# Performance work log

Hardware: AMD Instinct MI355X
Metric: run time of the kernel (lower is better)

## Reference

```python
import jax, jax.numpy as jnp
import numpy as np

NH = 16  # matches init kwarg nh


def setup_inputs() -> dict:
    key = jax.random.key(0)
    k1, k2 = jax.random.split(key)
    b, S, T = 4, 4096, 4096
    x = jax.random.normal(k1, (b, S, 1), dtype=jnp.float32)
    coords_rel = jax.random.normal(k2, (2, b, S, T), dtype=jnp.float32)
    return {"x": x, "coords_rel": coords_rel}


def reference(x, coords_rel):
    # coords_rel: [2, b, S, T]; x: [b, S, 1]
    d = jnp.sqrt(coords_rel[0] ** 2 + coords_rel[1] ** 2)            # [b, S, T]
    # torch.topk(d, NH, dim=1, largest=False): smallest NH along source dim, ascending
    neg_vals, idx = jax.lax.top_k(jnp.transpose(-d, (0, 2, 1)), NH)  # [b, T, NH]
    dist_abs = jnp.transpose(-neg_vals, (0, 2, 1))                   # [b, NH, T]
    indices = jnp.transpose(idx, (0, 2, 1))                          # [b, NH, T]
    b, nh, t = dist_abs.shape
    w = 1.0 / (dist_abs + 1e-15) ** 2                                # [b, nh, t]
    denom = w.sum(axis=2)                                            # [b, nh] (sum over t, as in source)
    # faithful reproduction of torch .view(t,b,nh) raw reinterpretation + broadcast divide + .view(b,t,nh)
    w = (w.reshape(t, b, nh) / denom).reshape(b, t, nh)              # [b, t, nh]
    S = x.shape[1]
    idx_btn = indices.reshape(b, t, nh)                              # raw reshape, matches torch .view
    # gather: out[i,j,k] = x[i, idx[i,j,k], 0]  (x.repeat over last dim makes all columns equal)
    xg = jnp.take_along_axis(jnp.broadcast_to(x, (b, S, nh)), idx_btn, axis=1)  # [b, t, nh]
    out = (xg * w).sum(axis=2)                                       # [b, t]
    return out[..., None]                                            # [b, t, 1]
```

## Files before the change

kernel.cpp:

```cpp
#include <hip/hip_runtime.h>

#define B_ 4
#define S_ 4096
#define T_ 4096
#define NH_ 16
#define CPB 32
#define CPW 2
#define ROWS 64
#define NTILE (S_ / ROWS)
#define LDSP 33
#define NCG (T_ / CPB)

typedef unsigned long long u64;

__global__ __launch_bounds__(1024, 8) void topk_scan(
    const float* __restrict__ coords,
    float* __restrict__ outW,
    int*   __restrict__ outI,
    float* __restrict__ partials)
{
    __shared__ float lds[2][2][ROWS * LDSP];
    __shared__ float red[16 * NH_];

    const int bid  = blockIdx.x;
    const int b    = bid >> 7;
    const int c0   = (bid & (NCG - 1)) * CPB;
    const int tid  = threadIdx.x;
    const int w    = tid >> 6;
    const int lane = tid & 63;

    const size_t plane = (size_t)B_ * S_ * T_;
    const int stid = tid & 511;
    const int srow = stid >> 3;
    const int scol = (stid & 7) * 4;
    const int pl   = (tid >= 512) ? 1 : 0;
    const float* gp = coords + (size_t)b * S_ * T_ + (size_t)srow * T_ + (c0 + scol)
                    + (pl ? plane : (size_t)0);
    float* w0 = &lds[0][pl][srow * LDSP + scol];
    float* w1 = &lds[1][pl][srow * LDSP + scol];

    float lv[CPW]; int li[CPW]; float tau[CPW];
#pragma unroll
    for (int cc = 0; cc < CPW; ++cc) {
        lv[cc]  = __int_as_float(0x7f800000);
        li[cc]  = 0;
        tau[cc] = __int_as_float(0x7f800000);
    }

    float4 r4 = *(const float4*)gp;
    w0[0] = r4.x; w0[1] = r4.y; w0[2] = r4.z; w0[3] = r4.w;
    r4 = *(const float4*)(gp + (size_t)ROWS * T_);
    __syncthreads();

#pragma unroll 1
    for (int k = 0; k < NTILE; ++k) {
        if (k + 1 < NTILE) {
            float* wb = (k & 1) ? w0 : w1;
            wb[0] = r4.x; wb[1] = r4.y; wb[2] = r4.z; wb[3] = r4.w;
        }
        if (k + 2 < NTILE)
            r4 = *(const float4*)(gp + (size_t)(k + 2) * ROWS * T_);

        const float* rb0 = lds[k & 1][0];
        const float* rb1 = lds[k & 1][1];
#pragma unroll
        for (int cc = 0; cc < CPW; ++cc) {
            const int col = w * CPW + cc;
            const float dx = rb0[lane * LDSP + col];
            const float dy = rb1[lane * LDSP + col];
            const float d2 = __fadd_rn(__fmul_rn(dx, dx), __fmul_rn(dy, dy));
            u64 m = __ballot(d2 < tau[cc]);
            while (m) {
                const int src = __ffsll(m) - 1;
                m &= m - 1;
                const float cd = __shfl(d2, src);
                const int   ci = k * ROWS + src;
                const unsigned pm = (unsigned)__ballot(lv[cc] <= cd) & 0xFFFFu;
                const int p = __popc(pm);
                const float uv = __shfl_up(lv[cc], 1);
                const int   ui = __shfl_up(li[cc], 1);
                const bool here  = (lane == p);
                const bool shift = (lane > p) && (lane < NH_);
                lv[cc] = here ? cd : (shift ? uv : lv[cc]);
                li[cc] = here ? ci : (shift ? ui : li[cc]);
                tau[cc] = __shfl(lv[cc], NH_ - 1);
                m &= __ballot(d2 < tau[cc]);
            }
        }
        __syncthreads();
    }

    float dsum = 0.f;
#pragma unroll
    for (int cc = 0; cc < CPW; ++cc) {
        const int t = c0 + w * CPW + cc;
        if (lane < NH_) {
            const float d = sqrtf(lv[cc]) + 1e-15f;
            const float wv = 1.0f / (d * d);
            outW[((size_t)b * T_ + t) * NH_ + lane] = wv;
            outI[((size_t)b * T_ + t) * NH_ + lane] = li[cc];
            dsum += wv;
        }
    }
    if (lane < NH_) red[w * NH_ + lane] = dsum;
    __syncthreads();
    if (tid < NH_) {
        float s = 0.f;
#pragma unroll
        for (int q = 0; q < 16; ++q) s += red[q * NH_ + tid];
        partials[(size_t)bid * NH_ + tid] = s;
    }
}

__global__ __launch_bounds__(128) void denom_reduce(
    const float* __restrict__ partials, float* __restrict__ denom)
{
    const int q = blockIdx.x;
    const int b = q >> 4, j = q & 15;
    const int g = threadIdx.x;
    __shared__ float sm[128];
    sm[g] = partials[(size_t)(b * NCG + g) * NH_ + j];
    __syncthreads();
    for (int s = 64; s > 0; s >>= 1) {
        if (g < s) sm[g] += sm[g + s];
        __syncthreads();
    }
    if (g == 0) denom[q] = sm[0];
}

__global__ __launch_bounds__(256) void out_kernel(
    const float* __restrict__ x,
    const float* __restrict__ outW,
    const int*   __restrict__ outI,
    const float* __restrict__ denom,
    float* __restrict__ out)
{
    const int gid = blockIdx.x * 256 + threadIdx.x;
    const int i = gid >> 12;
    const int j = gid & 4095;
    const int ih = j >> 8;
    const size_t base = ((size_t)i * T_ + (size_t)(j & 255) * NH_) * NH_ + ih;
    const int dq = (j & 3) * NH_;
    float acc = 0.f;
#pragma unroll
    for (int k = 0; k < NH_; ++k) {
        float w  = outW[base + (size_t)k * NH_];
        int   id = outI[base + (size_t)k * NH_];
        acc += x[i * S_ + id] * w / denom[dq + k];
    }
    out[gid] = acc;
}

extern "C" void kernel_launch(void* const* d_in, const int* in_sizes, int n_in,
                              void* d_out, int out_size, void* d_ws, size_t ws_size,
                              hipStream_t stream) {
    const float* x      = (const float*)d_in[0];
    const float* coords = (const float*)d_in[1];
    float* out = (float*)d_out;

    float* outW     = (float*)d_ws;
    int*   outI     = (int*)(outW + (size_t)B_ * T_ * NH_);
    float* partials = (float*)(outI + (size_t)B_ * T_ * NH_);
    float* denom    = partials + (size_t)(B_ * NCG) * NH_;

    topk_scan   <<<B_ * NCG,      1024, 0, stream>>>(coords, outW, outI, partials);
    denom_reduce<<<64,            128,  0, stream>>>(partials, denom);
    out_kernel  <<<B_ * T_ / 256, 256,  0, stream>>>(x, outW, outI, denom, out);
}
```

Baseline: 152.1 us.

## Stream coordinate tiles into LDS via direct global_load_lds with 4-buffer pipeline

Replaces the register-staged double-buffered copy of coordinate tiles with direct global-to-LDS loads (global_load_lds), using a 4-deep ring buffer and prefetch distance of two tiles with explicit vmcnt waits. The padded LDS layout is replaced with an XOR-swizzled layout to avoid bank conflicts, and one barrier per iteration is removed. It aims to cut VGPR staging traffic and hide global load latency, but it relies on the ring depth and a single barrier for correctness, and it raises LDS use per block.

```diff
diff --git a/kernel.cpp b/kernel.cpp
--- a/kernel.cpp
+++ b/kernel.cpp
@@ -7,11 +7,13 @@
 #define CPB 32
 #define CPW 2
 #define ROWS 64
-#define NTILE (S_ / ROWS)
-#define LDSP 33
+#define NT (S_ / ROWS)
+#define NBUF 4
 #define NCG (T_ / CPB)
 
 typedef unsigned long long u64;
+typedef const float __attribute__((address_space(1)))* gas1f;
+typedef float __attribute__((address_space(3)))* las3f;
 
 __global__ __launch_bounds__(1024, 8) void topk_scan(
     const float* __restrict__ coords,
@@ -19,7 +21,7 @@
     int*   __restrict__ outI,
     float* __restrict__ partials)
 {
-    __shared__ float lds[2][2][ROWS * LDSP];
+    __shared__ float lds[NBUF * 2 * ROWS * CPB];
     __shared__ float red[16 * NH_];
 
     const int bid  = blockIdx.x;
@@ -30,14 +32,10 @@
     const int lane = tid & 63;
 
     const size_t plane = (size_t)B_ * S_ * T_;
-    const int stid = tid & 511;
-    const int srow = stid >> 3;
-    const int scol = (stid & 7) * 4;
-    const int pl   = (tid >= 512) ? 1 : 0;
-    const float* gp = coords + (size_t)b * S_ * T_ + (size_t)srow * T_ + (c0 + scol)
-                    + (pl ? plane : (size_t)0);
-    float* w0 = &lds[0][pl][srow * LDSP + scol];
-    float* w1 = &lds[1][pl][srow * LDSP + scol];
+    const int srow   = ((w & 7) << 3) + (lane >> 3);
+    const int schunk = (lane & 7) ^ (lane >> 3);
+    const float* gtile = coords + (size_t)(w >> 3) * plane
+                       + ((size_t)b * S_ + srow) * T_ + (c0 + schunk * 4);
 
     float lv[CPW]; int li[CPW]; float tau[CPW];
 #pragma unroll
@@ -47,27 +45,32 @@
         tau[cc] = __int_as_float(0x7f800000);
     }
 
-    float4 r4 = *(const float4*)gp;
-    w0[0] = r4.x; w0[1] = r4.y; w0[2] = r4.z; w0[3] = r4.w;
-    r4 = *(const float4*)(gp + (size_t)ROWS * T_);
-    __syncthreads();
+#define ISSUE(kk) do {                                                         \
+    const float* gsrc_ = gtile + (size_t)(kk) * ROWS * T_;                     \
+    las3f ldst_ = (las3f)((char*)lds + (((kk) & 3) << 14) + (w << 10));        \
+    __builtin_amdgcn_global_load_lds((gas1f)gsrc_, ldst_, 16, 0, 0);           \
+} while (0)
+
+    ISSUE(0);
+    ISSUE(1);
 
 #pragma unroll 1
-    for (int k = 0; k < NTILE; ++k) {
-        if (k + 1 < NTILE) {
-            float* wb = (k & 1) ? w0 : w1;
-            wb[0] = r4.x; wb[1] = r4.y; wb[2] = r4.z; wb[3] = r4.w;
-        }
-        if (k + 2 < NTILE)
-            r4 = *(const float4*)(gp + (size_t)(k + 2) * ROWS * T_);
+    for (int k = 0; k < NT; ++k) {
+        if (k + 2 < NT) ISSUE(k + 2);
+        if (k + 2 < NT)      asm volatile("s_waitcnt vmcnt(2)" ::: "memory");
+        else if (k + 1 < NT) asm volatile("s_waitcnt vmcnt(1)" ::: "memory");
+        else                 asm volatile("s_waitcnt vmcnt(0)" ::: "memory");
+        __builtin_amdgcn_sched_barrier(0);
+        __builtin_amdgcn_s_barrier();
+        __builtin_amdgcn_sched_barrier(0);
 
-        const float* rb0 = lds[k & 1][0];
-        const float* rb1 = lds[k & 1][1];
+        const float* rb = lds + ((k & 3) << 12);
 #pragma unroll
         for (int cc = 0; cc < CPW; ++cc) {
-            const int col = w * CPW + cc;
-            const float dx = rb0[lane * LDSP + col];
-            const float dy = rb1[lane * LDSP + col];
+            const int c  = w * CPW + cc;
+            const int sw = (((c >> 2) ^ (lane & 7)) << 2) + (c & 3);
+            const float dx = rb[(lane << 5) + sw];
+            const float dy = rb[2048 + (lane << 5) + sw];
             const float d2 = __fadd_rn(__fmul_rn(dx, dx), __fmul_rn(dy, dy));
             u64 m = __ballot(d2 < tau[cc]);
             while (m) {
@@ -87,8 +90,8 @@
                 m &= __ballot(d2 < tau[cc]);
             }
         }
-        __syncthreads();
     }
+#undef ISSUE
 
     float dsum = 0.f;
 #pragma unroll
```

Measured after the change: 159.2 us. 4.7% more time.
